# Optimization experiments

Measured on AMD Instinct MI355X. Metric: run time of the kernel, lower is better.

The kernel has to match this reference:

```python
import jax, jax.numpy as jnp
import numpy as np

B, T, C, H = 4, 2048, 1024, 16
D = C // H  # head_size = 64


def setup_inputs() -> dict:
    key = jax.random.key(0)
    ks = jax.random.split(key, 9)
    s = 1.0 / np.sqrt(C)
    inp = {
        "x": jax.random.normal(ks[0], (B, T, C), dtype=jnp.float32),
        "mask": jnp.tril(jnp.ones((1, 1, T, T), dtype=jnp.int32)),
        "Wq": jax.random.uniform(ks[1], (C, C), jnp.float32, -s, s),
        "bq": jax.random.uniform(ks[2], (C,), jnp.float32, -s, s),
        "Wk": jax.random.uniform(ks[3], (C, C), jnp.float32, -s, s),
        "bk": jax.random.uniform(ks[4], (C,), jnp.float32, -s, s),
        "Wv": jax.random.uniform(ks[5], (C, C), jnp.float32, -s, s),
        "bv": jax.random.uniform(ks[6], (C,), jnp.float32, -s, s),
        "Wp": jax.random.uniform(ks[7], (C, C), jnp.float32, -s, s),
        "bp": jax.random.uniform(ks[8], (C,), jnp.float32, -s, s),
    }
    return inp


def reference(x, mask, Wq, bq, Wk, bk, Wv, bv, Wp, bp):
    # q/k/v projections, reshape to [B, H, T, D]
    def heads(h):
        return h.reshape(B, T, H, D).transpose(0, 2, 1, 3)

    q = heads(x @ Wq + bq)
    k = heads(x @ Wk + bk)
    v = heads(x @ Wv + bv)

    scale = 1.0 / jnp.sqrt(jnp.float32(D))
    att = jnp.einsum("bhtd,bhsd->bhts", q, k) * scale  # [B,H,T,T]
    att = jnp.where(mask == 0, jnp.float32(-jnp.inf), att)
    att = jax.nn.softmax(att, axis=-1)
    # dropout p=0.0 (eval): identity
    y = jnp.einsum("bhts,bhsd->bhtd", att, v)  # [B,H,T,D]
    y = y.transpose(0, 2, 1, 3).reshape(B, T, C)
    return y @ Wp + bp
```

## Files before the change

### kernel.cpp

```cpp
#include <hip/hip_runtime.h>
#include <stdint.h>


#define B_ 4
#define T_ 2048
#define C_ 1024
#define H_ 16
#define D_ 64
#define M_ (B_ * T_)

typedef __attribute__((ext_vector_type(8))) short short8;
typedef __attribute__((ext_vector_type(4))) float f32x4;
typedef __attribute__((ext_vector_type(16))) float f32x16;
typedef __attribute__((ext_vector_type(4))) unsigned short ushort4v;

__device__ __forceinline__ unsigned short f2bf(float f) {
  union { float f; uint32_t u; } v; v.f = f;
  return (unsigned short)((v.u + 0x7fffu + ((v.u >> 16) & 1u)) >> 16);
}

__device__ __forceinline__ uint32_t cvt_pk_bf16(float lo, float hi) {
  uint32_t r;
  asm("v_cvt_pk_bf16_f32 %0, %1, %2" : "=v"(r) : "v"(lo), "v"(hi));
  return r;
}

__device__ __forceinline__ void gload_lds16(const unsigned short* g, unsigned short* l) {
  __builtin_amdgcn_global_load_lds(
      (const __attribute__((address_space(1))) void*)g,
      (__attribute__((address_space(3))) void*)l, 16, 0, 0);
}

__global__ __launch_bounds__(256) void cast_x_kernel(const float* __restrict__ in,
                                                     unsigned short* __restrict__ out) {
  int i = blockIdx.x * 256 + threadIdx.x;
  f32x4 v = ((const f32x4*)in)[i];
  ushort4v o;
  o[0] = f2bf(v[0]); o[1] = f2bf(v[1]); o[2] = f2bf(v[2]); o[3] = f2bf(v[3]);
  ((ushort4v*)out)[i] = o;
}

__global__ __launch_bounds__(256) void transpose_w_kernel(const float* __restrict__ W,
                                                          unsigned short* __restrict__ Wt) {
  __shared__ float tile[32][33];
  const int tx = threadIdx.x & 31;
  const int ty = threadIdx.x >> 5;
  const int n0 = blockIdx.x * 32;
  const int k0 = blockIdx.y * 32;
#pragma unroll
  for (int j = 0; j < 4; ++j)
    tile[ty + j * 8][tx] = W[(size_t)(k0 + ty + j * 8) * C_ + n0 + tx];
  __syncthreads();
#pragma unroll
  for (int j = 0; j < 4; ++j)
    Wt[(size_t)(n0 + ty + j * 8) * C_ + k0 + tx] = f2bf(tile[tx][ty + j * 8]);
}

__global__ __launch_bounds__(256) void gemm_bt_kernel(
    const unsigned short* __restrict__ A, const unsigned short* __restrict__ Bt,
    const float* __restrict__ b0, const float* __restrict__ b1, const float* __restrict__ b2,
    void* __restrict__ o0, void* __restrict__ o1, void* __restrict__ o2,
    int M, int N, int K, int mode) {
  __shared__ unsigned short As[128 * 32];
  __shared__ unsigned short Bs[128 * 32];

  const int tid = threadIdx.x;
  const int wv = tid >> 6;
  const int ln = tid & 63;
  const int mtiles = M >> 7;
  const int bm = blockIdx.x % mtiles;
  const int bn = blockIdx.x / mtiles;
  const int brow = bm << 7;
  const int bcol = bn << 7;

  const int wr = wv >> 1, wc = wv & 1;
  const int lo16 = ln & 15, hi4 = ln >> 4;
  const int srow = ln >> 2;
  const int scol = (ln & 3) << 3;

  f32x4 acc[4][4];
#pragma unroll
  for (int m = 0; m < 4; ++m)
#pragma unroll
    for (int n = 0; n < 4; ++n) acc[m][n] = (f32x4){0.f, 0.f, 0.f, 0.f};

  for (int k0 = 0; k0 < K; k0 += 32) {
#pragma unroll
    for (int j = 0; j < 2; ++j) {
      const int r = j * 64 + wv * 16 + srow;
      gload_lds16(A + (size_t)(brow + r) * K + k0 + scol, &As[(j * 64 + wv * 16) * 32]);
      gload_lds16(Bt + (size_t)(bcol + r) * K + k0 + scol, &Bs[(j * 64 + wv * 16) * 32]);
    }
    __syncthreads();
    short8 af[4], bfr[4];
#pragma unroll
    for (int m = 0; m < 4; ++m)
      af[m] = *(const short8*)(&As[(wr * 64 + m * 16 + lo16) * 32 + hi4 * 8]);
#pragma unroll
    for (int n = 0; n < 4; ++n)
      bfr[n] = *(const short8*)(&Bs[(wc * 64 + n * 16 + lo16) * 32 + hi4 * 8]);
#pragma unroll
    for (int m = 0; m < 4; ++m)
#pragma unroll
      for (int n = 0; n < 4; ++n)
        acc[m][n] = __builtin_amdgcn_mfma_f32_16x16x32_bf16(af[m], bfr[n], acc[m][n], 0, 0, 0);
    __syncthreads();
  }

  const float SCALE_Q = 0.125f * 1.44269504f;
#pragma unroll
  for (int m = 0; m < 4; ++m) {
#pragma unroll
    for (int n = 0; n < 4; ++n) {
      const int rl = brow + wr * 64 + m * 16 + hi4 * 4;
      const int cgc = bcol + wc * 64 + n * 16 + lo16;
      if (mode == 2) {
        const float bias = b0[cgc];
#pragma unroll
        for (int r = 0; r < 4; ++r)
          ((float*)o0)[(size_t)(rl + r) * N + cgc] = acc[m][n][r] + bias;
      } else {
        const int which = cgc >> 10;
        const int cc = cgc & 1023;
        const float bias = ((which == 0) ? b0 : (which == 1) ? b1 : b2)[cc];
        const int h = cc >> 6, d = cc & 63;
#pragma unroll
        for (int r = 0; r < 4; ++r) {
          const int R = rl + r;
          const int bb = R >> 11, t = R & (T_ - 1);
          const int bh = bb * H_ + h;
          float val = acc[m][n][r] + bias;
          if (which == 0) val *= SCALE_Q;
          if (which == 2)
            ((unsigned short*)o2)[((size_t)bh * D_ + d) * T_ + t] = f2bf(val);
          else
            ((unsigned short*)((which == 0) ? o0 : o1))[((size_t)bh * T_ + t) * D_ + d] = f2bf(val);
        }
      }
    }
  }
}

__global__ __launch_bounds__(256) void attn_kernel(
    const unsigned short* __restrict__ Q, const unsigned short* __restrict__ Kb,
    const unsigned short* __restrict__ Vt, unsigned short* __restrict__ Y) {
  __shared__ unsigned short Ks[2][64 * 64];

  const int blk = blockIdx.x;
  const int xcd = blk & 7;
  const int j = blk >> 3;
  const int bh = xcd * 8 + (j & 7);
  const int qt = 15 - (j >> 3);
  const int wv = threadIdx.x >> 6;
  const int ln = threadIdx.x & 63;
  const int q31 = ln & 31;
  const int hi = ln >> 5;
  const int r0 = qt * 128 + wv * 32;

  const unsigned short* kp = Kb + (size_t)bh * T_ * D_;
  const unsigned short* vp = Vt + (size_t)bh * D_ * T_;

  const int sr = ln >> 3;
  const int scc = ln & 7;
  const int krow = wv * 16;

  const unsigned short* qp = Q + ((size_t)bh * T_ + r0) * D_;
  short8 qf[4];
#pragma unroll
  for (int kd = 0; kd < 4; ++kd)
    qf[kd] = *(const short8*)(qp + (size_t)q31 * D_ + kd * 16 + hi * 8);

  f32x16 o0, o1;
#pragma unroll
  for (int r = 0; r < 16; ++r) { o0[r] = 0.f; o1[r] = 0.f; }
  float mr = -1e38f, lr = 0.f;

  auto stage = [&](int b, int s0) {
#pragma unroll
    for (int jj = 0; jj < 2; ++jj) {
      const int r = krow + jj * 8 + sr;
      const int cs = (scc ^ (r & 7)) << 3;
      gload_lds16(kp + (size_t)(s0 + r) * D_ + cs, &Ks[b][(krow + jj * 8) * 64]);
    }
  };

  const int nt = 2 * qt + 2;
  const int it_last = (r0 + 31) >> 6;
  stage(0, 0);
  __syncthreads();
  int buf = 0;

  for (int it = 0; it < nt; ++it) {
    const int s0 = it << 6;
    if (it + 1 < nt) stage(buf ^ 1, s0 + 64);

    if (it <= it_last) {
      short8 vfr0[4], vfr1[4];
      const unsigned short* vb0 = vp + (size_t)q31 * T_ + s0 + hi * 8;
#pragma unroll
      for (int ks = 0; ks < 4; ++ks) {
        vfr0[ks] = *(const short8*)(vb0 + ks * 16);
        vfr1[ks] = *(const short8*)(vb0 + (size_t)32 * T_ + ks * 16);
      }

      f32x16 sa0, sa1;
#pragma unroll
      for (int r = 0; r < 16; ++r) { sa0[r] = 0.f; sa1[r] = 0.f; }
#pragma unroll
      for (int kd = 0; kd < 4; ++kd) {
        const short8 kf0 =
            *(const short8*)(&Ks[buf][q31 * 64 + (((2 * kd + hi) ^ (q31 & 7)) << 3)]);
        sa0 = __builtin_amdgcn_mfma_f32_32x32x16_bf16(kf0, qf[kd], sa0, 0, 0, 0);
      }
#pragma unroll
      for (int kd = 0; kd < 4; ++kd) {
        const int row = 32 + q31;
        const short8 kf1 =
            *(const short8*)(&Ks[buf][row * 64 + (((2 * kd + hi) ^ (row & 7)) << 3)]);
        sa1 = __builtin_amdgcn_mfma_f32_32x32x16_bf16(kf1, qf[kd], sa1, 0, 0, 0);
      }

      if (it == it_last) {
        const int qg = r0 + q31;
#pragma unroll
        for (int r = 0; r < 16; ++r) {
          const int sl = (r & 3) + ((r >> 2) << 3) + hi * 4;
          if (s0 + sl > qg) sa0[r] = -1e38f;
          if (s0 + 32 + sl > qg) sa1[r] = -1e38f;
        }
      }

      float pm = -1e38f;
#pragma unroll
      for (int r = 0; r < 16; ++r) pm = fmaxf(pm, fmaxf(sa0[r], sa1[r]));
      pm = fmaxf(pm, __shfl_xor(pm, 32));
      if (__any(pm > mr + 8.0f)) {
        const float mn = fmaxf(mr, pm);
        const float alpha = exp2f(mr - mn);
        mr = mn;
        lr *= alpha;
#pragma unroll
        for (int r = 0; r < 16; ++r) { o0[r] *= alpha; o1[r] *= alpha; }
      }
      float rsa = 0.f, rsb = 0.f;
#pragma unroll
      for (int r = 0; r < 16; ++r) {
        const float p0 = exp2f(sa0[r] - mr);
        const float p1 = exp2f(sa1[r] - mr);
        sa0[r] = p0; sa1[r] = p1;
        rsa += p0; rsb += p1;
      }
      float rs = rsa + rsb;
      rs += __shfl_xor(rs, 32);
      lr += rs;

      uint32_t pk[16];
#pragma unroll
      for (int u = 0; u < 4; ++u)
#pragma unroll
        for (int vp2 = 0; vp2 < 2; ++vp2) {
          pk[2 * u + vp2]     = cvt_pk_bf16(sa0[4 * u + 2 * vp2], sa0[4 * u + 2 * vp2 + 1]);
          pk[8 + 2 * u + vp2] = cvt_pk_bf16(sa1[4 * u + 2 * vp2], sa1[4 * u + 2 * vp2 + 1]);
        }

#pragma unroll
      for (int ks = 0; ks < 4; ++ks) {
        const uint32_t x0 = hi ? pk[4 * ks + 2] : pk[4 * ks + 0];
        const uint32_t x1 = hi ? pk[4 * ks + 3] : pk[4 * ks + 1];
        const uint32_t y0 = hi ? pk[4 * ks + 0] : pk[4 * ks + 2];
        const uint32_t y1 = hi ? pk[4 * ks + 1] : pk[4 * ks + 3];
        const uint32_t g0 = (uint32_t)__shfl_xor((int)y0, 32);
        const uint32_t g1 = (uint32_t)__shfl_xor((int)y1, 32);
        union { uint32_t w[4]; short8 v; } pf;
        pf.w[0] = hi ? g0 : x0;
        pf.w[1] = hi ? g1 : x1;
        pf.w[2] = hi ? x0 : g0;
        pf.w[3] = hi ? x1 : g1;
        o0 = __builtin_amdgcn_mfma_f32_32x32x16_bf16(vfr0[ks], pf.v, o0, 0, 0, 0);
        o1 = __builtin_amdgcn_mfma_f32_32x32x16_bf16(vfr1[ks], pf.v, o1, 0, 0, 0);
      }
    }
    __syncthreads();
    buf ^= 1;
  }

  const int b = bh >> 4, h = bh & 15;
  const float inv = 1.f / lr;
  const int t = r0 + q31;
  unsigned short* yrow = Y + ((size_t)(b * T_ + t)) * C_ + h * 64;
#pragma unroll
  for (int u = 0; u < 4; ++u) {
    union { uint32_t w[2]; ushort4v v; } w0, w1;
    w0.w[0] = cvt_pk_bf16(o0[4 * u + 0] * inv, o0[4 * u + 1] * inv);
    w0.w[1] = cvt_pk_bf16(o0[4 * u + 2] * inv, o0[4 * u + 3] * inv);
    w1.w[0] = cvt_pk_bf16(o1[4 * u + 0] * inv, o1[4 * u + 1] * inv);
    w1.w[1] = cvt_pk_bf16(o1[4 * u + 2] * inv, o1[4 * u + 3] * inv);
    *(ushort4v*)(yrow + u * 8 + hi * 4) = w0.v;
    *(ushort4v*)(yrow + 32 + u * 8 + hi * 4) = w1.v;
  }
}

extern "C" void kernel_launch(void* const* d_in, const int* in_sizes, int n_in,
                              void* d_out, int out_size, void* d_ws, size_t ws_size,
                              hipStream_t stream) {
  const float* x  = (const float*)d_in[0];
  const float* Wq = (const float*)d_in[2];
  const float* bq = (const float*)d_in[3];
  const float* Wk = (const float*)d_in[4];
  const float* bk = (const float*)d_in[5];
  const float* Wv = (const float*)d_in[6];
  const float* bv = (const float*)d_in[7];
  const float* Wp = (const float*)d_in[8];
  const float* bp = (const float*)d_in[9];
  float* out = (float*)d_out;

  uint8_t* ws = (uint8_t*)d_ws;
  if (ws_size < (76u << 20)) return;
  unsigned short* xb  = (unsigned short*)(ws);
  unsigned short* wqT = (unsigned short*)(ws + (16u << 20));
  unsigned short* wkT = (unsigned short*)(ws + (18u << 20));
  unsigned short* wvT = (unsigned short*)(ws + (20u << 20));
  unsigned short* wpT = (unsigned short*)(ws + (22u << 20));
  unsigned short* qb  = (unsigned short*)(ws + (24u << 20));
  unsigned short* kb  = (unsigned short*)(ws + (40u << 20));
  unsigned short* vtb = (unsigned short*)(ws + (56u << 20));

  cast_x_kernel<<<(M_ * C_ / 4) / 256, 256, 0, stream>>>(x, xb);
  dim3 tg(32, 32);
  transpose_w_kernel<<<tg, 256, 0, stream>>>(Wq, wqT);
  transpose_w_kernel<<<tg, 256, 0, stream>>>(Wk, wkT);
  transpose_w_kernel<<<tg, 256, 0, stream>>>(Wv, wvT);
  transpose_w_kernel<<<tg, 256, 0, stream>>>(Wp, wpT);

  gemm_bt_kernel<<<(M_ / 128) * (3 * C_ / 128), 256, 0, stream>>>(
      xb, wqT, bq, bk, bv, qb, kb, vtb, M_, 3 * C_, C_, 3);

  attn_kernel<<<B_ * H_ * (T_ / 128), 256, 0, stream>>>(qb, kb, vtb, xb);

  gemm_bt_kernel<<<(M_ / 128) * (C_ / 128), 256, 0, stream>>>(
      xb, wpT, bp, nullptr, nullptr, out, nullptr, nullptr, M_, C_, C_, 2);
}
```

Before: 238.2 us.

## Use 32x32 MFMA tiles, XOR-swizzled LDS, and XCD-aware block remap in GEMM

```diff
diff --git a/kernel.cpp b/kernel.cpp
--- a/kernel.cpp
+++ b/kernel.cpp
@@ -60,7 +60,7 @@
     const unsigned short* __restrict__ A, const unsigned short* __restrict__ Bt,
     const float* __restrict__ b0, const float* __restrict__ b1, const float* __restrict__ b2,
     void* __restrict__ o0, void* __restrict__ o1, void* __restrict__ o2,
-    int M, int N, int K, int mode) {
+    int M, int N, int K, int mode, int nblk) {
   __shared__ unsigned short As[128 * 32];
   __shared__ unsigned short Bs[128 * 32];
 
@@ -68,68 +68,86 @@
   const int wv = tid >> 6;
   const int ln = tid & 63;
   const int mtiles = M >> 7;
-  const int bm = blockIdx.x % mtiles;
-  const int bn = blockIdx.x / mtiles;
+  const int cpx = nblk >> 3;
+  const int sw = (blockIdx.x & 7) * cpx + (blockIdx.x >> 3);
+  const int bm = sw % mtiles;
+  const int bn = sw / mtiles;
   const int brow = bm << 7;
   const int bcol = bn << 7;
 
   const int wr = wv >> 1, wc = wv & 1;
-  const int lo16 = ln & 15, hi4 = ln >> 4;
+  const int lo32 = ln & 31, hi2 = ln >> 5;
   const int srow = ln >> 2;
-  const int scol = (ln & 3) << 3;
-
-  f32x4 acc[4][4];
-#pragma unroll
-  for (int m = 0; m < 4; ++m)
-#pragma unroll
-    for (int n = 0; n < 4; ++n) acc[m][n] = (f32x4){0.f, 0.f, 0.f, 0.f};
+  const int sch = ln & 3;
+
+  f32x16 acc[2][2];
+#pragma unroll
+  for (int m = 0; m < 2; ++m)
+#pragma unroll
+    for (int n = 0; n < 2; ++n)
+#pragma unroll
+      for (int r = 0; r < 16; ++r) acc[m][n][r] = 0.f;
 
   for (int k0 = 0; k0 < K; k0 += 32) {
 #pragma unroll
     for (int j = 0; j < 2; ++j) {
       const int r = j * 64 + wv * 16 + srow;
-      gload_lds16(A + (size_t)(brow + r) * K + k0 + scol, &As[(j * 64 + wv * 16) * 32]);
-      gload_lds16(Bt + (size_t)(bcol + r) * K + k0 + scol, &Bs[(j * 64 + wv * 16) * 32]);
+      const int cs = (sch ^ (r & 3)) << 3;
+      gload_lds16(A + (size_t)(brow + r) * K + k0 + cs, &As[(j * 64 + wv * 16) * 32]);
+      gload_lds16(Bt + (size_t)(bcol + r) * K + k0 + cs, &Bs[(j * 64 + wv * 16) * 32]);
     }
     __syncthreads();
-    short8 af[4], bfr[4];
-#pragma unroll
-    for (int m = 0; m < 4; ++m)
-      af[m] = *(const short8*)(&As[(wr * 64 + m * 16 + lo16) * 32 + hi4 * 8]);
-#pragma unroll
-    for (int n = 0; n < 4; ++n)
-      bfr[n] = *(const short8*)(&Bs[(wc * 64 + n * 16 + lo16) * 32 + hi4 * 8]);
-#pragma unroll
-    for (int m = 0; m < 4; ++m)
-#pragma unroll
-      for (int n = 0; n < 4; ++n)
-        acc[m][n] = __builtin_amdgcn_mfma_f32_16x16x32_bf16(af[m], bfr[n], acc[m][n], 0, 0, 0);
+    short8 af[2][2], bfr[2][2];
+#pragma unroll
+    for (int mi = 0; mi < 2; ++mi) {
+      const int row = wr * 64 + mi * 32 + lo32;
+#pragma unroll
+      for (int ks = 0; ks < 2; ++ks)
+        af[mi][ks] = *(const short8*)(&As[row * 32 + (((ks * 2 + hi2) ^ (row & 3)) << 3)]);
+    }
+#pragma unroll
+    for (int ni = 0; ni < 2; ++ni) {
+      const int row = wc * 64 + ni * 32 + lo32;
+#pragma unroll
+      for (int ks = 0; ks < 2; ++ks)
+        bfr[ni][ks] = *(const short8*)(&Bs[row * 32 + (((ks * 2 + hi2) ^ (row & 3)) << 3)]);
+    }
+#pragma unroll
+    for (int mi = 0; mi < 2; ++mi)
+#pragma unroll
+      for (int ni = 0; ni < 2; ++ni)
+#pragma unroll
+        for (int ks = 0; ks < 2; ++ks)
+          acc[mi][ni] = __builtin_amdgcn_mfma_f32_32x32x16_bf16(af[mi][ks], bfr[ni][ks],
+                                                                acc[mi][ni], 0, 0, 0);
     __syncthreads();
   }
 
   const float SCALE_Q = 0.125f * 1.44269504f;
 #pragma unroll
-  for (int m = 0; m < 4; ++m) {
-#pragma unroll
-    for (int n = 0; n < 4; ++n) {
-      const int rl = brow + wr * 64 + m * 16 + hi4 * 4;
-      const int cgc = bcol + wc * 64 + n * 16 + lo16;
+  for (int mi = 0; mi < 2; ++mi) {
+#pragma unroll
+    for (int ni = 0; ni < 2; ++ni) {
+      const int rowbase = brow + wr * 64 + mi * 32 + 4 * hi2;
+      const int cgc = bcol + wc * 64 + ni * 32 + lo32;
       if (mode == 2) {
         const float bias = b0[cgc];
 #pragma unroll
-        for (int r = 0; r < 4; ++r)
-          ((float*)o0)[(size_t)(rl + r) * N + cgc] = acc[m][n][r] + bias;
+        for (int reg = 0; reg < 16; ++reg) {
+          const int row = rowbase + (reg & 3) + 8 * (reg >> 2);
+          ((float*)o0)[(size_t)row * N + cgc] = acc[mi][ni][reg] + bias;
+        }
       } else {
         const int which = cgc >> 10;
         const int cc = cgc & 1023;
         const float bias = ((which == 0) ? b0 : (which == 1) ? b1 : b2)[cc];
         const int h = cc >> 6, d = cc & 63;
 #pragma unroll
-        for (int r = 0; r < 4; ++r) {
-          const int R = rl + r;
+        for (int reg = 0; reg < 16; ++reg) {
+          const int R = rowbase + (reg & 3) + 8 * (reg >> 2);
           const int bb = R >> 11, t = R & (T_ - 1);
           const int bh = bb * H_ + h;
-          float val = acc[m][n][r] + bias;
+          float val = acc[mi][ni][reg] + bias;
           if (which == 0) val *= SCALE_Q;
           if (which == 2)
             ((unsigned short*)o2)[((size_t)bh * D_ + d) * T_ + t] = f2bf(val);
@@ -332,11 +350,17 @@
   transpose_w_kernel<<<tg, 256, 0, stream>>>(Wv, wvT);
   transpose_w_kernel<<<tg, 256, 0, stream>>>(Wp, wpT);
 
-  gemm_bt_kernel<<<(M_ / 128) * (3 * C_ / 128), 256, 0, stream>>>(
-      xb, wqT, bq, bk, bv, qb, kb, vtb, M_, 3 * C_, C_, 3);
+  {
+    const int nblk = (M_ / 128) * (3 * C_ / 128);
+    gemm_bt_kernel<<<nblk, 256, 0, stream>>>(
+        xb, wqT, bq, bk, bv, qb, kb, vtb, M_, 3 * C_, C_, 3, nblk);
+  }
 
   attn_kernel<<<B_ * H_ * (T_ / 128), 256, 0, stream>>>(qb, kb, vtb, xb);
 
-  gemm_bt_kernel<<<(M_ / 128) * (C_ / 128), 256, 0, stream>>>(
-      xb, wpT, bp, nullptr, nullptr, out, nullptr, nullptr, M_, C_, C_, 2);
-}
+  {
+    const int nblk = (M_ / 128) * (C_ / 128);
+    gemm_bt_kernel<<<nblk, 256, 0, stream>>>(
+        xb, wpT, bp, nullptr, nullptr, out, nullptr, nullptr, M_, C_, C_, 2, nblk);
+  }
+}
```

Measured after the change: 275.6 us. 15.7% more time.
